# Optimization experiments

Hardware: AMD Instinct MI355X
Metric: run time of the kernel (lower is better)

Reference implementation:

```python
import jax, jax.numpy as jnp
import numpy as np

HIDDEN = 2048
NH = 32       # num query heads
NKV = 8       # num kv heads
D = 64        # head_dim = hidden // NH
BSX, BSY = 32, 32  # block sizes


def setup_inputs() -> dict:
    key = jax.random.key(0)
    ks = jax.random.split(key, 5)
    B, L = 2, 4096  # L = x_dim * y_dim
    w = lambda k, sh, fan: jax.random.normal(k, sh, jnp.float32) * (fan ** -0.5)
    return {
        "hidden_states": jax.random.normal(ks[0], (B, L, HIDDEN), jnp.float32),
        "Wq": w(ks[1], (HIDDEN, NH * D), HIDDEN),
        "Wk": w(ks[2], (HIDDEN, NKV * D), HIDDEN),
        "Wv": w(ks[3], (HIDDEN, NKV * D), HIDDEN),
        "Wo": w(ks[4], (NH * D, HIDDEN), NH * D),
        "x_dim": 64,
        "y_dim": 64,
    }


def _block_split(x, B, bnx, bny, h):
    # einops: 'b (bnx bsx bny bsy) (h d) -> (b bnx bny) (bsx bsy) h d'
    x = x.reshape(B, bnx, BSX, bny, BSY, h, D)
    x = x.transpose(0, 1, 3, 2, 4, 5, 6)  # b bnx bny bsx bsy h d
    return x.reshape(B * bnx * bny, BSX * BSY, h, D)


def reference(hidden_states, Wq, Wk, Wv, Wo, x_dim, y_dim):
    B, L, _ = hidden_states.shape
    bnx, bny = x_dim // BSX, y_dim // BSY
    q = _block_split(hidden_states @ Wq, B, bnx, bny, NH)   # [nb, T, NH, D]
    k = _block_split(hidden_states @ Wk, B, bnx, bny, NKV)  # [nb, T, NKV, D]
    v = _block_split(hidden_states @ Wv, B, bnx, bny, NKV)
    g = NH // NKV  # GQA groups: query head i attends kv head i // g
    k = jnp.repeat(k, g, axis=2)
    v = jnp.repeat(v, g, axis=2)
    scores = jnp.einsum('nqhd,nkhd->nhqk', q, k) * (D ** -0.5)
    p = jax.nn.softmax(scores, axis=-1)
    o = jnp.einsum('nhqk,nkhd->nqhd', p, v)  # [nb, T, NH, D]
    # Faithful to the torch code: plain reshape (does NOT invert the block rearrange)
    o = o.reshape(B, L, NH * D)
    return o @ Wo
```

## Files before the change

### kernel.cpp

```cpp
#include <hip/hip_runtime.h>

typedef __bf16 bf16_t;
typedef __bf16 bf16x8 __attribute__((ext_vector_type(8)));
typedef __bf16 bf16x4 __attribute__((ext_vector_type(4)));
typedef float f32x4 __attribute__((ext_vector_type(4)));
typedef float f32x16 __attribute__((ext_vector_type(16)));
typedef short s16x4 __attribute__((ext_vector_type(4)));
typedef short s16x8 __attribute__((ext_vector_type(8)));
typedef unsigned u32x2 __attribute__((ext_vector_type(2)));

#define MFMA16(A_, B_, C_) __builtin_amdgcn_mfma_f32_16x16x32_bf16((A_), (B_), (C_), 0, 0, 0)
#define MFMA32(A_, B_, C_) __builtin_amdgcn_mfma_f32_32x32x16_bf16((A_), (B_), (C_), 0, 0, 0)

#define QSC 0.18033688011112042f

#if __has_builtin(__builtin_amdgcn_exp2f)
#define EXP2F(x) __builtin_amdgcn_exp2f(x)
#else
#define EXP2F(x) exp2f(x)
#endif

__device__ __forceinline__ void gload_lds16(const bf16_t* g, bf16_t* l) {
  __builtin_amdgcn_global_load_lds(
      (const __attribute__((address_space(1))) void*)g,
      (__attribute__((address_space(3))) void*)l, 16, 0, 0);
}

__device__ __forceinline__ unsigned cvt_pk_bf16(float a, float b) {
  unsigned r;
  asm("v_cvt_pk_bf16_f32 %0, %1, %2" : "=v"(r) : "v"(a), "v"(b));
  return r;
}

__device__ __forceinline__ s16x4 tr_b16(const bf16_t* p) {
  s16x4 d;
  unsigned off = (unsigned)(size_t)(const __attribute__((address_space(3))) bf16_t*)p;
  asm volatile("ds_read_b64_tr_b16 %0, %1" : "=v"(d) : "v"(off));
  return d;
}

union B128 { s16x8 s; bf16x8 b; };

#define DSR(PTR, U)                                                           \
  do {                                                                        \
    unsigned _o = (unsigned)(size_t)                                          \
        (const __attribute__((address_space(3))) bf16_t*)(PTR);               \
    asm volatile("ds_read_b128 %0, %1" : "=v"((U).s) : "v"(_o));              \
  } while (0)

#define DSR_OFS(BASEV, OFFSTR, U)                                             \
  asm volatile("ds_read_b128 %0, %1 offset:" OFFSTR                           \
               : "=v"((U).s) : "v"(BASEV))

__device__ __forceinline__ void swap32(unsigned a, unsigned b, int hi,
                                       unsigned& ra, unsigned& rb) {
#if __has_builtin(__builtin_amdgcn_permlane32_swap)
  u32x2 r = __builtin_amdgcn_permlane32_swap(b, a, false, false);
  rb = r[0]; ra = r[1];
#else
  unsigned bx = (unsigned)__shfl_xor((int)b, 32);
  unsigned ax = (unsigned)__shfl_xor((int)a, 32);
  ra = hi ? a : bx;
  rb = hi ? ax : b;
#endif
}

__global__ __launch_bounds__(256) void k_convert(const float* __restrict__ in,
                                                 bf16_t* __restrict__ out, int n4) {
  int i = blockIdx.x * 256 + threadIdx.x;
  if (i >= n4) return;
  float4 v = ((const float4*)in)[i];
  bf16x4 o;
  o[0] = (__bf16)v.x; o[1] = (__bf16)v.y; o[2] = (__bf16)v.z; o[3] = (__bf16)v.w;
  *(bf16x4*)(out + (size_t)i * 4) = o;
}

__global__ __launch_bounds__(256) void k_transpose(const float* __restrict__ in,
                                                   bf16_t* __restrict__ out, int R, int C) {
  __shared__ float tile[64][65];
  int tx = threadIdx.x & 63;
  int ty = threadIdx.x >> 6;
  int bc = blockIdx.x * 64;
  int br = blockIdx.y * 64;
#pragma unroll
  for (int i = ty; i < 64; i += 4)
    tile[i][tx] = in[(size_t)(br + i) * C + bc + tx];
  __syncthreads();
#pragma unroll
  for (int i = ty; i < 64; i += 4)
    out[(size_t)(bc + i) * R + br + tx] = (bf16_t)tile[tx][i];
}

__device__ __forceinline__ int permrow(int r) {
  int b  = r >> 12;
  int l  = r & 4095;
  int ix = (l >> 11) & 1;
  int sx = (l >> 6) & 31;
  int iy = (l >> 5) & 1;
  int sy = l & 31;
  return (b << 12) + (ix << 11) + (iy << 10) + (sx << 5) + sy;
}

#define SBAR __builtin_amdgcn_sched_barrier(0)

#define LA(K_) (lds + (K_)*24576)
#define LB(K_) (lds + (K_)*24576 + 16384)

__global__ __launch_bounds__(512, 2) void k_gemmA(
    const bf16_t* __restrict__ A,
    const bf16_t* __restrict__ B0, const bf16_t* __restrict__ B1,
    const bf16_t* __restrict__ B2,
    bf16_t* __restrict__ Cq, bf16_t* __restrict__ Ck, bf16_t* __restrict__ Cv) {
  extern __shared__ bf16_t lds[];

  int bid = blockIdx.x;
  int s = bid >> 3;
  int tm = (bid & 7) * 4 + s / 24;
  int tn = s % 24;

  const bf16_t* Bp;
  int brow;
  if (tn < 16)      { Bp = B0; brow = tn << 7; }
  else if (tn < 20) { Bp = B1; brow = (tn - 16) << 7; }
  else              { Bp = B2; brow = (tn - 20) << 7; }

  int tid = threadIdx.x;
  int lane = tid & 63;
  int w = tid >> 6;
  int wm = w >> 1, wn = w & 1;
  int g16 = lane >> 4, cl = lane & 15;
  int swz8 = (cl & 7) << 3;
  int wofs = w << 9;

  int srow = tid >> 3;
  int lc = (((tid & 7) ^ (srow & 7)) << 3);
  const bf16_t* aBt = A + (size_t)(tm * 256 + srow) * 2048 + lc;
  const bf16_t* bBt = Bp + (size_t)(brow + srow) * 2048 + lc;

  unsigned ldsb = (unsigned)(size_t)(__attribute__((address_space(3))) bf16_t*)lds;
  unsigned arow0 = (unsigned)((wm * 64 + cl) * 128 + (((g16 * 8) ^ swz8) << 1));
  unsigned arow1 = (unsigned)((wm * 64 + cl) * 128 + ((((32 + g16 * 8)) ^ swz8) << 1));
  unsigned brow0 = (unsigned)(32768 + (wn * 64 + cl) * 128 + (((g16 * 8) ^ swz8) << 1));
  unsigned brow1 = (unsigned)(32768 + (wn * 64 + cl) * 128 + ((((32 + g16 * 8)) ^ swz8) << 1));
  unsigned a0[3], a1[3], b0[3], b1[3];
#pragma unroll
  for (int kk = 0; kk < 3; ++kk) {
    a0[kk] = ldsb + kk * 49152 + arow0;
    a1[kk] = ldsb + kk * 49152 + arow1;
    b0[kk] = ldsb + kk * 49152 + brow0;
    b1[kk] = ldsb + kk * 49152 + brow1;
  }

#define GA_STAGE(K2_)                                                          \
  _Pragma("unroll") for (int rr = 0; rr < 4; ++rr)                             \
    gload_lds16(aBt + (size_t)(rr * 64) * 2048, LA(K2_) + rr * 4096 + wofs);   \
  _Pragma("unroll") for (int rr = 0; rr < 2; ++rr)                             \
    gload_lds16(bBt + (size_t)(rr * 64) * 2048, LB(K2_) + rr * 4096 + wofs);   \
  aBt += 64; bBt += 64;

#define GA_MFMA_ALL                                                            \
  _Pragma("unroll") for (int kk = 0; kk < 2; ++kk)                             \
    _Pragma("unroll") for (int m = 0; m < 4; ++m)                              \
      _Pragma("unroll") for (int ni = 0; ni < 4; ++ni)                         \
        acc[m][ni] = MFMA16(af[m][kk].b, bfr[ni][kk].b, acc[m][ni]);

#define GA_BODY(K_, K2_, VMSTR_, DOSTAGE_)                                     \
  {                                                                            \
    B128 af[4][2], bfr[4][2];                                                  \
    asm volatile("s_waitcnt vmcnt(" VMSTR_ ")" ::: "memory");                  \
    __builtin_amdgcn_s_barrier();                                              \
    DSR_OFS(b0[K_], "0",    bfr[0][0]); DSR_OFS(b0[K_], "2048", bfr[1][0]);    \
    DSR_OFS(b0[K_], "4096", bfr[2][0]); DSR_OFS(b0[K_], "6144", bfr[3][0]);    \
    DSR_OFS(b1[K_], "0",    bfr[0][1]); DSR_OFS(b1[K_], "2048", bfr[1][1]);    \
    DSR_OFS(b1[K_], "4096", bfr[2][1]); DSR_OFS(b1[K_], "6144", bfr[3][1]);    \
    DSR_OFS(a0[K_], "0",    af[0][0]);  DSR_OFS(a0[K_], "2048", af[1][0]);     \
    DSR_OFS(a0[K_], "4096", af[2][0]);  DSR_OFS(a0[K_], "6144", af[3][0]);     \
    DSR_OFS(a1[K_], "0",    af[0][1]);  DSR_OFS(a1[K_], "2048", af[1][1]);     \
    DSR_OFS(a1[K_], "4096", af[2][1]);  DSR_OFS(a1[K_], "6144", af[3][1]);     \
    if (DOSTAGE_) { GA_STAGE(K2_); }                                           \
    asm volatile("s_waitcnt lgkmcnt(0)" ::: "memory");                         \
    SBAR;                                                                      \
    __builtin_amdgcn_s_setprio(1);                                             \
    GA_MFMA_ALL;                                                               \
    __builtin_amdgcn_s_setprio(0);                                             \
  }

  f32x4 acc[4][4];
#pragma unroll
  for (int i = 0; i < 4; ++i)
#pragma unroll
    for (int j = 0; j < 4; ++j) acc[i][j] = (f32x4)(0.0f);

  GA_STAGE(0);
  GA_STAGE(1);

  for (int t3 = 0; t3 < 30; t3 += 3) {
    GA_BODY(0, 2, "6", 1);
    GA_BODY(1, 0, "6", 1);
    GA_BODY(2, 1, "6", 1);
  }
  GA_BODY(0, 2, "6", 0);
  GA_BODY(1, 0, "0", 0);

#pragma unroll
  for (int mi = 0; mi < 4; ++mi) {
#pragma unroll
    for (int rr = 0; rr < 4; ++rr) {
      int r = tm * 256 + wm * 64 + mi * 16 + g16 * 4 + rr;
      int rp = permrow(r);
#pragma unroll
      for (int ni = 0; ni < 4; ++ni) {
        int c = tn * 128 + wn * 64 + ni * 16 + cl;
        float v = acc[mi][ni][rr];
        if (c < 2048)      Cq[(size_t)rp * 2048 + c] = (bf16_t)(v * QSC);
        else if (c < 2560) Ck[(size_t)rp * 512 + (c - 2048)] = (bf16_t)v;
        else               Cv[(size_t)rp * 512 + (c - 2560)] = (bf16_t)v;
      }
    }
  }
}

#define LSLOT(B_, M_, H_) (lds + (((B_)*4 + (M_)*2 + (H_)) << 13))

#define STAGE_A(BUF, HF, T)                                                     \
  gload_lds16(aB + (size_t)((HF)*128) * 2048 + (T)*64, LSLOT(BUF, 0, HF) + wofs); \
  gload_lds16(aB + (size_t)((HF)*128 + 64) * 2048 + (T)*64,                     \
              LSLOT(BUF, 0, HF) + wofs + 4096);

#define STAGE_B(BUF, HF, T)                                                     \
  gload_lds16(bB + (size_t)((HF)*128) * 2048 + (T)*64, LSLOT(BUF, 1, HF) + wofs); \
  gload_lds16(bB + (size_t)((HF)*128 + 64) * 2048 + (T)*64,                     \
              LSLOT(BUF, 1, HF) + wofs + 4096);

#define LOAD_A(BUF, Q)                                                          \
  { const bf16_t* Ah = LSLOT(BUF, 0, wm) + ((Q)*32 + cl) * 64;                  \
    DSR(Ah + ((g16 * 8) ^ swz8), af[0][0]);                                     \
    DSR(Ah + ((32 + g16 * 8) ^ swz8), af[0][1]);                                \
    DSR(Ah + 1024 + ((g16 * 8) ^ swz8), af[1][0]);                              \
    DSR(Ah + 1024 + ((32 + g16 * 8) ^ swz8), af[1][1]); }

#define LOAD_B(BUF)                                                             \
  { const bf16_t* Bh = LSLOT(BUF, 1, wn >> 1);                                  \
    _Pragma("unroll") for (int ni = 0; ni < 4; ++ni) {                          \
      const bf16_t* Br = Bh + ((wn & 1) * 64 + ni * 16 + cl) * 64;              \
      DSR(Br + ((g16 * 8) ^ swz8), bfr[ni][0]);                                 \
      DSR(Br + ((32 + g16 * 8) ^ swz8), bfr[ni][1]); } }

#define MFMA_QUAD(Q)                                                            \
  _Pragma("unroll") for (int kk = 0; kk < 2; ++kk)                              \
    _Pragma("unroll") for (int ni = 0; ni < 4; ++ni) {                          \
      acc[2*(Q)][ni]   = MFMA16(af[0][kk].b, bfr[ni][kk].b, acc[2*(Q)][ni]);    \
      acc[2*(Q)+1][ni] = MFMA16(af[1][kk].b, bfr[ni][kk].b, acc[2*(Q)+1][ni]); }

#define PH_MID(VM4)                                                             \
  if (VM4) asm volatile("s_waitcnt vmcnt(4)" ::: "memory");                     \
  __builtin_amdgcn_s_barrier();                                                 \
  asm volatile("s_waitcnt lgkmcnt(0)" ::: "memory");                            \
  SBAR;                                                                         \
  __builtin_amdgcn_s_setprio(1);

#define PH_END                                                                  \
  SBAR;                                                                         \
  __builtin_amdgcn_s_setprio(0);                                                \
  __builtin_amdgcn_s_barrier();

__global__ __launch_bounds__(512, 2) void k_gemmB(
    const bf16_t* __restrict__ A, const bf16_t* __restrict__ B0,
    float* __restrict__ Cf) {
  extern __shared__ bf16_t lds[];

  int bid = blockIdx.x;
  int s = bid >> 3;
  int tm = (bid & 7) * 4 + (s >> 3);
  int tn = s & 7;
  const bf16_t* Bp = B0;
  int brow = tn << 8;

  int tid = threadIdx.x;
  int lane = tid & 63;
  int w = tid >> 6;
  int wm = w >> 2, wn = w & 3;
  int g16 = lane >> 4, cl = lane & 15;
  int swz8 = (cl & 7) << 3;
  int wofs = w << 9;

  int srow = tid >> 3;
  int lc = (((tid & 7) ^ (srow & 7)) << 3);
  const bf16_t* aB = A + (size_t)(tm * 256 + srow) * 2048 + lc;
  const bf16_t* bB = Bp + (size_t)(brow + srow) * 2048 + lc;

  f32x4 acc[8][4];
#pragma unroll
  for (int i = 0; i < 8; ++i)
#pragma unroll
    for (int j = 0; j < 4; ++j) acc[i][j] = (f32x4)(0.0f);

  STAGE_A(0, 0, 0); STAGE_A(0, 1, 0);
  STAGE_B(0, 0, 0); STAGE_B(0, 1, 0);
  STAGE_B(1, 0, 1); STAGE_B(1, 1, 1);
  asm volatile("s_waitcnt vmcnt(4)" ::: "memory");
  __builtin_amdgcn_s_barrier();

  for (int it2 = 0; it2 < 16; ++it2) {
    int t1 = 2 * it2 + 1;
    int tf = 2 * it2 + 2; if (tf > 31) tf = 31;
    int tg = 2 * it2 + 3; if (tg > 31) tg = 31;
    B128 af[2][2], bfr[4][2];
    STAGE_A(1, 0, t1);
    LOAD_B(0); LOAD_A(0, 0);
    PH_MID(0); MFMA_QUAD(0); PH_END;
    STAGE_A(1, 1, t1);
    LOAD_A(0, 1);
    PH_MID(0); MFMA_QUAD(1); PH_END;
    STAGE_B(0, 0, tf);
    LOAD_A(0, 2);
    PH_MID(0); MFMA_QUAD(2); PH_END;
    STAGE_B(0, 1, tf);
    LOAD_A(0, 3);
    PH_MID(1); MFMA_QUAD(3); PH_END;
    STAGE_A(0, 0, tf);
    LOAD_B(1); LOAD_A(1, 0);
    PH_MID(0); MFMA_QUAD(0); PH_END;
    STAGE_A(0, 1, tf);
    LOAD_A(1, 1);
    PH_MID(0); MFMA_QUAD(1); PH_END;
    STAGE_B(1, 0, tg);
    LOAD_A(1, 2);
    PH_MID(0); MFMA_QUAD(2); PH_END;
    STAGE_B(1, 1, tg);
    LOAD_A(1, 3);
    PH_MID(1); MFMA_QUAD(3); PH_END;
  }

#pragma unroll
  for (int mi = 0; mi < 8; ++mi) {
#pragma unroll
    for (int rr = 0; rr < 4; ++rr) {
      int r = tm * 256 + wm * 128 + mi * 16 + g16 * 4 + rr;
#pragma unroll
      for (int ni = 0; ni < 4; ++ni) {
        int c = tn * 256 + wn * 64 + ni * 16 + cl;
        Cf[(size_t)r * 2048 + c] = acc[mi][ni][rr];
      }
    }
  }
}

__global__ __launch_bounds__(256, 2) void k_attn(
    const bf16_t* __restrict__ Qp, const bf16_t* __restrict__ Kp,
    const bf16_t* __restrict__ Vp, bf16_t* __restrict__ O) {
  int bid = blockIdx.x;
  int qc = bid & 7;
  int h  = (bid >> 3) & 31;
  int n  = bid >> 8;
  int kvh = h >> 2;

  __shared__ bf16_t buf[2][8192];

  int tid = threadIdx.x, lane = tid & 63, w = tid >> 6;
  int l31 = lane & 31, hi = lane >> 5;
  int qrow_blk = n * 1024 + qc * 128;
  bf16_t* base = &buf[0][0];

#pragma unroll
  for (int r = 0; r < 4; ++r) {
    int ql = r * 32 + (tid >> 3);
    int cs = (tid & 7) << 4;
    int lc = (cs ^ ((ql & 7) << 4)) >> 1;
    gload_lds16(Qp + (size_t)(qrow_blk + ql) * 2048 + h * 64 + lc,
                base + r * 2048 + w * 512);
  }
  __syncthreads();
  bf16x8 qf[4];
  {
    int q = w * 32 + l31;
    const bf16_t* qrow = base + q * 64;
    int sw = (q & 7) << 4;
#pragma unroll
    for (int c = 0; c < 4; ++c)
      qf[c] = *(const bf16x8*)(qrow + (((c * 32 + hi * 16) ^ sw) >> 1));
  }
  __syncthreads();

  f32x16 oacc0 = (f32x16)(0.0f), oacc1 = (f32x16)(0.0f);
  float m_run = -1e30f, l_run = 0.0f;

  auto stageKV = [&](int t) {
    bf16_t* bp = &buf[t & 1][0];
    int kvb = n * 1024 + t * 64;
#pragma unroll
    for (int r = 0; r < 2; ++r) {
      int kv = r * 32 + (tid >> 3);
      int cs = (tid & 7) << 4;
      int lc = (cs ^ ((kv & 7) << 4)) >> 1;
      gload_lds16(Kp + (size_t)(kvb + kv) * 512 + kvh * 64 + lc,
                  bp + r * 2048 + w * 512);
    }
#pragma unroll
    for (int r = 0; r < 2; ++r) {
      int slot = r * 256 + tid;
      int sub = slot >> 3;
      int kb = sub >> 2, db = sub & 3;
      int j = (slot >> 1) & 3, hf = slot & 1;
      gload_lds16(Vp + (size_t)(kvb + kb * 4 + j) * 512 + kvh * 64 + db * 16 + hf * 8,
                  bp + 4096 + r * 2048 + w * 512);
    }
  };

  stageKV(0);
  for (int t = 0; t < 16; ++t) {
    __syncthreads();
    if (t < 15) stageKV(t + 1);
    const bf16_t* bp = &buf[t & 1][0];
    const bf16_t* Vs = bp + 4096;

#pragma unroll
    for (int s = 0; s < 2; ++s) {
      f32x16 st = (f32x16)(0.0f);
      {
        int kv = s * 32 + l31;
        const bf16_t* krow = bp + kv * 64;
        int sw = (kv & 7) << 4;
#pragma unroll
        for (int c = 0; c < 4; ++c) {
          bf16x8 kf = *(const bf16x8*)(krow + (((c * 32 + hi * 16) ^ sw) >> 1));
          st = MFMA32(kf, qf[c], st);
        }
      }
      float p0 = fmaxf(fmaxf(st[0], st[1]), st[2]);
      float p1 = fmaxf(fmaxf(st[3], st[4]), st[5]);
      float p2 = fmaxf(fmaxf(st[6], st[7]), st[8]);
      float p3 = fmaxf(fmaxf(st[9], st[10]), st[11]);
      float p4 = fmaxf(fmaxf(st[12], st[13]), st[14]);
      float pmax = fmaxf(fmaxf(fmaxf(p0, p1), p2),
                         fmaxf(fmaxf(p3, p4), st[15]));
      pmax = fmaxf(pmax, __shfl_xor(pmax, 32));
      if (!__all(pmax <= m_run + 11.0f)) {
        float mnew = fmaxf(m_run, pmax);
        float resc = EXP2F(m_run - mnew);
        l_run *= resc;
#pragma unroll
        for (int e = 0; e < 16; ++e) { oacc0[e] *= resc; oacc1[e] *= resc; }
        m_run = mnew;
      }
      float rs = 0.0f;
      unsigned pw[8];
#pragma unroll
      for (int u = 0; u < 8; ++u) {
        float q0 = EXP2F(st[2 * u] - m_run);
        float q1 = EXP2F(st[2 * u + 1] - m_run);
        rs += q0 + q1;
        pw[u] = cvt_pk_bf16(q0, q1);
      }
      rs += __shfl_xor(rs, 32);
      l_run += rs;

#pragma unroll
      for (int c = 0; c < 2; ++c) {
        unsigned w2, w0, w3, w1;
        swap32(pw[c * 4 + 2], pw[c * 4 + 0], hi, w2, w0);
        swap32(pw[c * 4 + 3], pw[c * 4 + 1], hi, w3, w1);
        union { unsigned u[4]; bf16x8 v; } pa;
        pa.u[0] = w0; pa.u[1] = w1; pa.u[2] = w2; pa.u[3] = w3;
        int kb0 = s * 8 + c * 4 + hi * 2;
        int dbl = l31 >> 4;
        int cc8 = (l31 & 15) * 4;
        const bf16_t* p00 = Vs + (kb0 * 4 + dbl) * 64 + cc8;
        const bf16_t* p01 = Vs + ((kb0 + 1) * 4 + dbl) * 64 + cc8;
        const bf16_t* p10 = Vs + (kb0 * 4 + 2 + dbl) * 64 + cc8;
        const bf16_t* p11 = Vs + ((kb0 + 1) * 4 + 2 + dbl) * 64 + cc8;
        s16x4 t00 = tr_b16(p00), t01 = tr_b16(p01);
        s16x4 t10 = tr_b16(p10), t11 = tr_b16(p11);
        asm volatile("s_waitcnt lgkmcnt(0)" ::: "memory");
        __builtin_amdgcn_sched_barrier(0);
        union { s16x4 s4[2]; bf16x8 v; } vf0, vf1;
        vf0.s4[0] = t00; vf0.s4[1] = t01;
        vf1.s4[0] = t10; vf1.s4[1] = t11;
        oacc0 = MFMA32(pa.v, vf0.v, oacc0);
        oacc1 = MFMA32(pa.v, vf1.v, oacc1);
      }
    }
  }

  float linv = 1.0f / l_run;
#pragma unroll
  for (int r = 0; r < 16; ++r) {
    int qrw = (r & 3) + 8 * (r >> 2) + 4 * hi;
    float li = __shfl(linv, qrw);
    size_t orow = (size_t)(qrow_blk + w * 32 + qrw) * 2048 + h * 64 + l31;
    O[orow]      = (bf16_t)(oacc0[r] * li);
    O[orow + 32] = (bf16_t)(oacc1[r] * li);
  }
}

extern "C" void kernel_launch(void* const* d_in, const int* in_sizes, int n_in,
                              void* d_out, int out_size, void* d_ws, size_t ws_size,
                              hipStream_t stream) {
  const float* X  = (const float*)d_in[0];
  const float* Wq = (const float*)d_in[1];
  const float* Wk = (const float*)d_in[2];
  const float* Wv = (const float*)d_in[3];
  const float* Wo = (const float*)d_in[4];
  float* out = (float*)d_out;

  char* ws = (char*)d_ws;
  const size_t MB = 1024 * 1024;
  bf16_t* Xb  = (bf16_t*)(ws + 0);
  bf16_t* WqT = (bf16_t*)(ws + 32 * MB);
  bf16_t* WkT = (bf16_t*)(ws + 40 * MB);
  bf16_t* WvT = (bf16_t*)(ws + 42 * MB);
  bf16_t* WoT = (bf16_t*)(ws + 44 * MB);
  bf16_t* Qp  = (bf16_t*)(ws + 52 * MB);
  bf16_t* Kp  = (bf16_t*)(ws + 84 * MB);
  bf16_t* Vp  = (bf16_t*)(ws + 92 * MB);
  bf16_t* Ob  = (bf16_t*)(ws + 100 * MB);

  hipFuncSetAttribute(reinterpret_cast<const void*>(&k_gemmA),
                      hipFuncAttributeMaxDynamicSharedMemorySize, 147456);
  hipFuncSetAttribute(reinterpret_cast<const void*>(&k_gemmB),
                      hipFuncAttributeMaxDynamicSharedMemorySize, 131072);

  k_convert<<<16384, 256, 0, stream>>>(X, Xb, 4194304);
  k_transpose<<<dim3(32, 32), 256, 0, stream>>>(Wq, WqT, 2048, 2048);
  k_transpose<<<dim3(8, 32), 256, 0, stream>>>(Wk, WkT, 2048, 512);
  k_transpose<<<dim3(8, 32), 256, 0, stream>>>(Wv, WvT, 2048, 512);
  k_transpose<<<dim3(32, 32), 256, 0, stream>>>(Wo, WoT, 2048, 2048);

  k_gemmA<<<768, 512, 147456, stream>>>(Xb, WqT, WkT, WvT, Qp, Kp, Vp);
  k_attn<<<2048, 256, 0, stream>>>(Qp, Kp, Vp, Ob);
  k_gemmB<<<256, 512, 131072, stream>>>(Ob, WoT, out);
}
```

Before: 320.6 us.

## Reuse triple-buffered QKV GEMM for output projection and interleave LDS reads with MFMAs

Templates the QKV GEMM kernel so it also serves the output projection, replacing the separate double-buffered 256x256-tile kernel with a 256x128-tile, three-stage pipeline launched on 512 blocks. It also reorders the A-fragment LDS reads and uses staged lgkmcnt waits, so MFMAs for each M row start as soon as their fragments arrive instead of after all reads finish. The smaller tile gives more blocks for the 256-block projection but lowers per-block data reuse.

Measured after the change: 321.3 us. Within noise of the previous version (+0.2%).

```diff
diff --git a/kernel.cpp b/kernel.cpp
--- a/kernel.cpp
+++ b/kernel.cpp
@@ -106,23 +106,30 @@
 #define LA(K_) (lds + (K_)*24576)
 #define LB(K_) (lds + (K_)*24576 + 16384)
 
-__global__ __launch_bounds__(512, 2) void k_gemmA(
+template <int MODE>
+__global__ __launch_bounds__(512, 2) void k_gemm15(
     const bf16_t* __restrict__ A,
     const bf16_t* __restrict__ B0, const bf16_t* __restrict__ B1,
     const bf16_t* __restrict__ B2,
-    bf16_t* __restrict__ Cq, bf16_t* __restrict__ Ck, bf16_t* __restrict__ Cv) {
+    bf16_t* __restrict__ Cq, bf16_t* __restrict__ Ck, bf16_t* __restrict__ Cv,
+    float* __restrict__ Cf) {
   extern __shared__ bf16_t lds[];
 
+  const int TN = (MODE == 0) ? 24 : 16;
   int bid = blockIdx.x;
   int s = bid >> 3;
-  int tm = (bid & 7) * 4 + s / 24;
-  int tn = s % 24;
+  int tm = (bid & 7) * 4 + s / TN;
+  int tn = s % TN;
 
   const bf16_t* Bp;
   int brow;
-  if (tn < 16)      { Bp = B0; brow = tn << 7; }
-  else if (tn < 20) { Bp = B1; brow = (tn - 16) << 7; }
-  else              { Bp = B2; brow = (tn - 20) << 7; }
+  if (MODE == 0) {
+    if (tn < 16)      { Bp = B0; brow = tn << 7; }
+    else if (tn < 20) { Bp = B1; brow = (tn - 16) << 7; }
+    else              { Bp = B2; brow = (tn - 20) << 7; }
+  } else {
+    Bp = B0; brow = tn << 7;
+  }
 
   int tid = threadIdx.x;
   int lane = tid & 63;
@@ -158,11 +165,10 @@
     gload_lds16(bBt + (size_t)(rr * 64) * 2048, LB(K2_) + rr * 4096 + wofs);   \
   aBt += 64; bBt += 64;
 
-#define GA_MFMA_ALL                                                            \
+#define GA_MFMA_M(M_)                                                          \
   _Pragma("unroll") for (int kk = 0; kk < 2; ++kk)                             \
-    _Pragma("unroll") for (int m = 0; m < 4; ++m)                              \
-      _Pragma("unroll") for (int ni = 0; ni < 4; ++ni)                         \
-        acc[m][ni] = MFMA16(af[m][kk].b, bfr[ni][kk].b, acc[m][ni]);
+    _Pragma("unroll") for (int ni = 0; ni < 4; ++ni)                           \
+      acc[M_][ni] = MFMA16(af[M_][kk].b, bfr[ni][kk].b, acc[M_][ni]);
 
 #define GA_BODY(K_, K2_, VMSTR_, DOSTAGE_)                                     \
   {                                                                            \
@@ -173,15 +179,24 @@
     DSR_OFS(b0[K_], "4096", bfr[2][0]); DSR_OFS(b0[K_], "6144", bfr[3][0]);    \
     DSR_OFS(b1[K_], "0",    bfr[0][1]); DSR_OFS(b1[K_], "2048", bfr[1][1]);    \
     DSR_OFS(b1[K_], "4096", bfr[2][1]); DSR_OFS(b1[K_], "6144", bfr[3][1]);    \
-    DSR_OFS(a0[K_], "0",    af[0][0]);  DSR_OFS(a0[K_], "2048", af[1][0]);     \
-    DSR_OFS(a0[K_], "4096", af[2][0]);  DSR_OFS(a0[K_], "6144", af[3][0]);     \
-    DSR_OFS(a1[K_], "0",    af[0][1]);  DSR_OFS(a1[K_], "2048", af[1][1]);     \
-    DSR_OFS(a1[K_], "4096", af[2][1]);  DSR_OFS(a1[K_], "6144", af[3][1]);     \
+    DSR_OFS(a0[K_], "0",    af[0][0]);  DSR_OFS(a1[K_], "0",    af[0][1]);     \
+    DSR_OFS(a0[K_], "2048", af[1][0]);  DSR_OFS(a1[K_], "2048", af[1][1]);     \
+    DSR_OFS(a0[K_], "4096", af[2][0]);  DSR_OFS(a1[K_], "4096", af[2][1]);     \
+    DSR_OFS(a0[K_], "6144", af[3][0]);  DSR_OFS(a1[K_], "6144", af[3][1]);     \
     if (DOSTAGE_) { GA_STAGE(K2_); }                                           \
+    asm volatile("s_waitcnt lgkmcnt(6)" ::: "memory");                         \
+    SBAR;                                                                      \
+    __builtin_amdgcn_s_setprio(1);                                             \
+    GA_MFMA_M(0);                                                              \
+    asm volatile("s_waitcnt lgkmcnt(4)" ::: "memory");                         \
+    SBAR;                                                                      \
+    GA_MFMA_M(1);                                                              \
+    asm volatile("s_waitcnt lgkmcnt(2)" ::: "memory");                         \
+    SBAR;                                                                      \
+    GA_MFMA_M(2);                                                              \
     asm volatile("s_waitcnt lgkmcnt(0)" ::: "memory");                         \
     SBAR;                                                                      \
-    __builtin_amdgcn_s_setprio(1);                                             \
-    GA_MFMA_ALL;                                                               \
+    GA_MFMA_M(3);                                                              \
     __builtin_amdgcn_s_setprio(0);                                             \
   }
 
@@ -207,140 +222,22 @@
 #pragma unroll
     for (int rr = 0; rr < 4; ++rr) {
       int r = tm * 256 + wm * 64 + mi * 16 + g16 * 4 + rr;
-      int rp = permrow(r);
-#pragma unroll
-      for (int ni = 0; ni < 4; ++ni) {
-        int c = tn * 128 + wn * 64 + ni * 16 + cl;
-        float v = acc[mi][ni][rr];
-        if (c < 2048)      Cq[(size_t)rp * 2048 + c] = (bf16_t)(v * QSC);
-        else if (c < 2560) Ck[(size_t)rp * 512 + (c - 2048)] = (bf16_t)v;
-        else               Cv[(size_t)rp * 512 + (c - 2560)] = (bf16_t)v;
-      }
-    }
-  }
-}
-
-#define LSLOT(B_, M_, H_) (lds + (((B_)*4 + (M_)*2 + (H_)) << 13))
-
-#define STAGE_A(BUF, HF, T)                                                     \
-  gload_lds16(aB + (size_t)((HF)*128) * 2048 + (T)*64, LSLOT(BUF, 0, HF) + wofs); \
-  gload_lds16(aB + (size_t)((HF)*128 + 64) * 2048 + (T)*64,                     \
-              LSLOT(BUF, 0, HF) + wofs + 4096);
-
-#define STAGE_B(BUF, HF, T)                                                     \
-  gload_lds16(bB + (size_t)((HF)*128) * 2048 + (T)*64, LSLOT(BUF, 1, HF) + wofs); \
-  gload_lds16(bB + (size_t)((HF)*128 + 64) * 2048 + (T)*64,                     \
-              LSLOT(BUF, 1, HF) + wofs + 4096);
-
-#define LOAD_A(BUF, Q)                                                          \
-  { const bf16_t* Ah = LSLOT(BUF, 0, wm) + ((Q)*32 + cl) * 64;                  \
-    DSR(Ah + ((g16 * 8) ^ swz8), af[0][0]);                                     \
-    DSR(Ah + ((32 + g16 * 8) ^ swz8), af[0][1]);                                \
-    DSR(Ah + 1024 + ((g16 * 8) ^ swz8), af[1][0]);                              \
-    DSR(Ah + 1024 + ((32 + g16 * 8) ^ swz8), af[1][1]); }
-
-#define LOAD_B(BUF)                                                             \
-  { const bf16_t* Bh = LSLOT(BUF, 1, wn >> 1);                                  \
-    _Pragma("unroll") for (int ni = 0; ni < 4; ++ni) {                          \
-      const bf16_t* Br = Bh + ((wn & 1) * 64 + ni * 16 + cl) * 64;              \
-      DSR(Br + ((g16 * 8) ^ swz8), bfr[ni][0]);                                 \
-      DSR(Br + ((32 + g16 * 8) ^ swz8), bfr[ni][1]); } }
-
-#define MFMA_QUAD(Q)                                                            \
-  _Pragma("unroll") for (int kk = 0; kk < 2; ++kk)                              \
-    _Pragma("unroll") for (int ni = 0; ni < 4; ++ni) {                          \
-      acc[2*(Q)][ni]   = MFMA16(af[0][kk].b, bfr[ni][kk].b, acc[2*(Q)][ni]);    \
-      acc[2*(Q)+1][ni] = MFMA16(af[1][kk].b, bfr[ni][kk].b, acc[2*(Q)+1][ni]); }
-
-#define PH_MID(VM4)                                                             \
-  if (VM4) asm volatile("s_waitcnt vmcnt(4)" ::: "memory");                     \
-  __builtin_amdgcn_s_barrier();                                                 \
-  asm volatile("s_waitcnt lgkmcnt(0)" ::: "memory");                            \
-  SBAR;                                                                         \
-  __builtin_amdgcn_s_setprio(1);
-
-#define PH_END                                                                  \
-  SBAR;                                                                         \
-  __builtin_amdgcn_s_setprio(0);                                                \
-  __builtin_amdgcn_s_barrier();
-
-__global__ __launch_bounds__(512, 2) void k_gemmB(
-    const bf16_t* __restrict__ A, const bf16_t* __restrict__ B0,
-    float* __restrict__ Cf) {
-  extern __shared__ bf16_t lds[];
-
-  int bid = blockIdx.x;
-  int s = bid >> 3;
-  int tm = (bid & 7) * 4 + (s >> 3);
-  int tn = s & 7;
-  const bf16_t* Bp = B0;
-  int brow = tn << 8;
-
-  int tid = threadIdx.x;
-  int lane = tid & 63;
-  int w = tid >> 6;
-  int wm = w >> 2, wn = w & 3;
-  int g16 = lane >> 4, cl = lane & 15;
-  int swz8 = (cl & 7) << 3;
-  int wofs = w << 9;
-
-  int srow = tid >> 3;
-  int lc = (((tid & 7) ^ (srow & 7)) << 3);
-  const bf16_t* aB = A + (size_t)(tm * 256 + srow) * 2048 + lc;
-  const bf16_t* bB = Bp + (size_t)(brow + srow) * 2048 + lc;
-
-  f32x4 acc[8][4];
-#pragma unroll
-  for (int i = 0; i < 8; ++i)
-#pragma unroll
-    for (int j = 0; j < 4; ++j) acc[i][j] = (f32x4)(0.0f);
-
-  STAGE_A(0, 0, 0); STAGE_A(0, 1, 0);
-  STAGE_B(0, 0, 0); STAGE_B(0, 1, 0);
-  STAGE_B(1, 0, 1); STAGE_B(1, 1, 1);
-  asm volatile("s_waitcnt vmcnt(4)" ::: "memory");
-  __builtin_amdgcn_s_barrier();
-
-  for (int it2 = 0; it2 < 16; ++it2) {
-    int t1 = 2 * it2 + 1;
-    int tf = 2 * it2 + 2; if (tf > 31) tf = 31;
-    int tg = 2 * it2 + 3; if (tg > 31) tg = 31;
-    B128 af[2][2], bfr[4][2];
-    STAGE_A(1, 0, t1);
-    LOAD_B(0); LOAD_A(0, 0);
-    PH_MID(0); MFMA_QUAD(0); PH_END;
-    STAGE_A(1, 1, t1);
-    LOAD_A(0, 1);
-    PH_MID(0); MFMA_QUAD(1); PH_END;
-    STAGE_B(0, 0, tf);
-    LOAD_A(0, 2);
-    PH_MID(0); MFMA_QUAD(2); PH_END;
-    STAGE_B(0, 1, tf);
-    LOAD_A(0, 3);
-    PH_MID(1); MFMA_QUAD(3); PH_END;
-    STAGE_A(0, 0, tf);
-    LOAD_B(1); LOAD_A(1, 0);
-    PH_MID(0); MFMA_QUAD(0); PH_END;
-    STAGE_A(0, 1, tf);
-    LOAD_A(1, 1);
-    PH_MID(0); MFMA_QUAD(1); PH_END;
-    STAGE_B(1, 0, tg);
-    LOAD_A(1, 2);
-    PH_MID(0); MFMA_QUAD(2); PH_END;
-    STAGE_B(1, 1, tg);
-    LOAD_A(1, 3);
-    PH_MID(1); MFMA_QUAD(3); PH_END;
-  }
-
-#pragma unroll
-  for (int mi = 0; mi < 8; ++mi) {
-#pragma unroll
-    for (int rr = 0; rr < 4; ++rr) {
-      int r = tm * 256 + wm * 128 + mi * 16 + g16 * 4 + rr;
-#pragma unroll
-      for (int ni = 0; ni < 4; ++ni) {
-        int c = tn * 256 + wn * 64 + ni * 16 + cl;
-        Cf[(size_t)r * 2048 + c] = acc[mi][ni][rr];
+      if (MODE == 0) {
+        int rp = permrow(r);
+#pragma unroll
+        for (int ni = 0; ni < 4; ++ni) {
+          int c = tn * 128 + wn * 64 + ni * 16 + cl;
+          float v = acc[mi][ni][rr];
+          if (c < 2048)      Cq[(size_t)rp * 2048 + c] = (bf16_t)(v * QSC);
+          else if (c < 2560) Ck[(size_t)rp * 512 + (c - 2048)] = (bf16_t)v;
+          else               Cv[(size_t)rp * 512 + (c - 2560)] = (bf16_t)v;
+        }
+      } else {
+#pragma unroll
+        for (int ni = 0; ni < 4; ++ni) {
+          int c = tn * 128 + wn * 64 + ni * 16 + cl;
+          Cf[(size_t)r * 2048 + c] = acc[mi][ni][rr];
+        }
       }
     }
   }
@@ -515,10 +412,10 @@
   bf16_t* Vp  = (bf16_t*)(ws + 92 * MB);
   bf16_t* Ob  = (bf16_t*)(ws + 100 * MB);
 
-  hipFuncSetAttribute(reinterpret_cast<const void*>(&k_gemmA),
+  hipFuncSetAttribute(reinterpret_cast<const void*>(&k_gemm15<0>),
                       hipFuncAttributeMaxDynamicSharedMemorySize, 147456);
-  hipFuncSetAttribute(reinterpret_cast<const void*>(&k_gemmB),
-                      hipFuncAttributeMaxDynamicSharedMemorySize, 131072);
+  hipFuncSetAttribute(reinterpret_cast<const void*>(&k_gemm15<1>),
+                      hipFuncAttributeMaxDynamicSharedMemorySize, 147456);
 
   k_convert<<<16384, 256, 0, stream>>>(X, Xb, 4194304);
   k_transpose<<<dim3(32, 32), 256, 0, stream>>>(Wq, WqT, 2048, 2048);
@@ -526,7 +423,9 @@
   k_transpose<<<dim3(8, 32), 256, 0, stream>>>(Wv, WvT, 2048, 512);
   k_transpose<<<dim3(32, 32), 256, 0, stream>>>(Wo, WoT, 2048, 2048);
 
-  k_gemmA<<<768, 512, 147456, stream>>>(Xb, WqT, WkT, WvT, Qp, Kp, Vp);
+  k_gemm15<0><<<768, 512, 147456, stream>>>(Xb, WqT, WkT, WvT, Qp, Kp, Vp,
+                                            nullptr);
   k_attn<<<2048, 256, 0, stream>>>(Qp, Kp, Vp, Ob);
-  k_gemmB<<<256, 512, 131072, stream>>>(Ob, WoT, out);
-}
+  k_gemm15<1><<<512, 512, 147456, stream>>>(Ob, WoT, nullptr, nullptr, nullptr,
+                                            nullptr, nullptr, out);
+}
```
